# Performance work log

Hardware: AMD Instinct MI355X
Metric: run time of the kernel (lower is better)

The kernel has to match this reference:

```python
import jax, jax.numpy as jnp
import numpy as np

B, C, Q = 16, 1024, 128
XD, YD = 64, 32
D, H, HID, L = 512, 8, 2048, 6
HD = D // H
NEG = -1e9


def setup_inputs() -> dict:
    key = jax.random.key(0)
    ks = jax.random.split(key, 12)
    rn = lambda k, shape, s: jax.random.normal(k, shape, jnp.float32) * s
    return {
        "x_c": rn(ks[0], (B, C, XD), 1.0),
        "y_c": rn(ks[1], (B, C, YD), 1.0),
        "x_q": rn(ks[2], (B, Q, XD), 1.0),
        "W_val": rn(ks[3], (XD + YD, D), (XD + YD) ** -0.5),
        "b_val": jnp.zeros((D,), jnp.float32),
        "q_emb": rn(ks[4], (D,), D ** -0.5),
        "in_proj_w": rn(ks[5], (L, 3 * D, D), D ** -0.5),
        "in_proj_b": jnp.zeros((L, 3 * D), jnp.float32),
        "out_w": rn(ks[6], (L, D, D), D ** -0.5),
        "out_b": jnp.zeros((L, D), jnp.float32),
        "ln1_g": jnp.ones((L, D), jnp.float32),
        "ln1_b": jnp.zeros((L, D), jnp.float32),
        "lin1_w": rn(ks[7], (L, HID, D), D ** -0.5),
        "lin1_b": jnp.zeros((L, HID), jnp.float32),
        "lin2_w": rn(ks[8], (L, D, HID), HID ** -0.5),
        "lin2_b": jnp.zeros((L, D), jnp.float32),
        "ln2_g": jnp.ones((L, D), jnp.float32),
        "ln2_b": jnp.zeros((L, D), jnp.float32),
        "W_head": rn(ks[9], (D, YD), D ** -0.5),
        "b_head": jnp.zeros((YD,), jnp.float32),
    }


def _layernorm(x, g, b):
    mu = x.mean(-1, keepdims=True)
    var = ((x - mu) ** 2).mean(-1, keepdims=True)
    return (x - mu) * jax.lax.rsqrt(var + 1e-5) * g + b


def _forward(x_c, y_c, x_q, W_val, b_val, q_emb, in_proj_w, in_proj_b, out_w,
             out_b, ln1_g, ln1_b, lin1_w, lin1_b, lin2_w, lin2_b, ln2_g, ln2_b,
             W_head, b_head):
    bsz, c_len, _ = x_c.shape
    q_len = x_q.shape[1]
    S = c_len + q_len
    # concat y onto x; queries get zero y placeholder
    xy_c = jnp.concatenate([x_c, y_c], axis=-1)
    xy_q = jnp.concatenate([x_q, jnp.zeros((bsz, q_len, y_c.shape[-1]), x_q.dtype)], axis=-1)
    xy = jnp.concatenate([xy_c, xy_q], axis=1) @ W_val + b_val          # [B,S,D]
    xy = xy.at[:, -q_len:].add(q_emb)
    # src_mask: no one may attend to query positions (last q_len keys)
    bias = jnp.where(jnp.arange(S) >= c_len, jnp.float32(NEG), jnp.float32(0.0))  # [S] key axis

    def layer(x, p):
        ipw, ipb, ow, ob, g1, b1, w1, bb1, w2, bb2, g2, b2 = p
        qkv = x @ ipw.T + ipb                                           # [B,S,3D]
        q, k, v = jnp.split(qkv, 3, axis=-1)
        heads = lambda t: t.reshape(bsz, S, H, HD).transpose(0, 2, 1, 3)  # [B,H,S,HD]
        q, k, v = heads(q), heads(k), heads(v)
        scores = jnp.einsum('bhqd,bhkd->bhqk', q, k) / np.float32(np.sqrt(HD)) + bias
        attn = jax.nn.softmax(scores, axis=-1)
        ctx = jnp.einsum('bhqk,bhkd->bhqd', attn, v)
        ctx = ctx.transpose(0, 2, 1, 3).reshape(bsz, S, D)
        x = _layernorm(x + ctx @ ow.T + ob, g1, b1)                     # post-norm
        ff = jax.nn.relu(x @ w1.T + bb1) @ w2.T + bb2
        x = _layernorm(x + ff, g2, b2)
        return x, None

    params = (in_proj_w, in_proj_b, out_w, out_b, ln1_g, ln1_b,
              lin1_w, lin1_b, lin2_w, lin2_b, ln2_g, ln2_b)
    x, _ = jax.lax.scan(layer, xy, params)
    return x[:, -q_len:] @ W_head + b_head                              # [B,Q,YD]


def reference(x_c, y_c, x_q, W_val, b_val, q_emb, in_proj_w, in_proj_b, out_w,
              out_b, ln1_g, ln1_b, lin1_w, lin1_b, lin2_w, lin2_b, ln2_g, ln2_b,
              W_head, b_head):
    return _forward(x_c, y_c, x_q, W_val, b_val, q_emb, in_proj_w, in_proj_b,
                    out_w, out_b, ln1_g, ln1_b, lin1_w, lin1_b, lin2_w, lin2_b,
                    ln2_g, ln2_b, W_head, b_head)
```

## Files before the change

kernel.cpp:

```cpp
#include <hip/hip_runtime.h>

#define B_   16
#define C_   1024
#define Q_   128
#define S_   1152
#define D_   512
#define H_   8
#define HID_ 2048
#define L_   6
#define M_   (B_*S_)
#define MQ_  (B_*Q_)
#define QSC_ 0.18033688011f

typedef short bf16x8 __attribute__((ext_vector_type(8)));
typedef float f32x4  __attribute__((ext_vector_type(4)));
#define MFMA16(a,b,c) __builtin_amdgcn_mfma_f32_16x16x32_bf16(a,b,c,0,0,0)

__device__ __forceinline__ unsigned short f2b(float f){
  union { float f; unsigned u; } v; v.f = f;
  return (unsigned short)((v.u + 0x7FFF + ((v.u >> 16) & 1)) >> 16);
}
__device__ __forceinline__ float b2f(unsigned short u){
  return __uint_as_float((unsigned)u << 16);
}
__device__ __forceinline__ void gload16(const void* g, void* l){
  __builtin_amdgcn_global_load_lds((const __attribute__((address_space(1))) void*)g,
                                   (__attribute__((address_space(3))) void*)l, 16, 0, 0);
}
__device__ __forceinline__ float waveSum(float v){
  #pragma unroll
  for (int o = 32; o > 0; o >>= 1) v += __shfl_down(v, o, 64);
  return v;
}

__global__ __launch_bounds__(256) void f2b_kernel(
    const float* __restrict__ in, unsigned short* __restrict__ out, int n4)
{
  int i = blockIdx.x*256 + threadIdx.x;
  for (; i < n4; i += gridDim.x*256) {
    float4 v = ((const float4*)in)[i];
    ushort4 o = { f2b(v.x), f2b(v.y), f2b(v.z), f2b(v.w) };
    ((ushort4*)out)[i] = o;
  }
}

__global__ __launch_bounds__(256) void f2bq_kernel(
    const float* __restrict__ in, unsigned short* __restrict__ out, int n4)
{
  int i = blockIdx.x*256 + threadIdx.x;
  for (; i < n4; i += gridDim.x*256) {
    const int row = (i >> 7) % 1536;
    const float s = (row < 512) ? QSC_ : 1.f;
    float4 v = ((const float4*)in)[i];
    ushort4 o = { f2b(v.x*s), f2b(v.y*s), f2b(v.z*s), f2b(v.w*s) };
    ((ushort4*)out)[i] = o;
  }
}

__global__ __launch_bounds__(256) void sbias_kernel(
    const float* __restrict__ in, float* __restrict__ out)
{
  int idx = blockIdx.x*256 + threadIdx.x;
  if (idx < L_*1536) {
    int j = idx % 1536;
    out[idx] = in[idx] * (j < 512 ? QSC_ : 1.f);
  }
}

__global__ __launch_bounds__(256) void packxy_kernel(
    const float* __restrict__ x_c, const float* __restrict__ y_c,
    const float* __restrict__ x_q, unsigned short* __restrict__ XY)
{
  int idx = blockIdx.x*256 + threadIdx.x;
  const int n = M_*128;
  for (; idx < n; idx += gridDim.x*256) {
    int row = idx >> 7, col = idx & 127;
    int bb = row / S_, s = row % S_;
    float v;
    if (col < 64) {
      v = (s < C_) ? x_c[((size_t)bb*C_ + s)*64 + col]
                   : x_q[((size_t)bb*Q_ + (s - C_))*64 + col];
    } else if (col < 96) {
      v = (s < C_) ? y_c[((size_t)bb*C_ + s)*32 + (col - 64)] : 0.f;
    } else if (col == 96) {
      v = 1.f;
    } else if (col == 97) {
      v = (s >= C_) ? 1.f : 0.f;
    } else v = 0.f;
    XY[idx] = f2b(v);
  }
}

__global__ __launch_bounds__(256) void wemb_kernel(
    const float* __restrict__ W_val, const float* __restrict__ b_val,
    const float* __restrict__ q_emb, unsigned short* __restrict__ Wemb)
{
  int idx = blockIdx.x*256 + threadIdx.x;
  int nn = idx >> 7, k = idx & 127;
  float v;
  if (k < 96)       v = W_val[k*D_ + nn];
  else if (k == 96) v = b_val[nn];
  else if (k == 97) v = q_emb[nn];
  else              v = 0.f;
  Wemb[idx] = f2b(v);
}

__global__ __launch_bounds__(256) void gatherq_kernel(
    const unsigned short* __restrict__ X, unsigned short* __restrict__ Xq)
{
  int row = blockIdx.x;
  int bb = row >> 7, qi = row & 127;
  const unsigned short* src = X + ((size_t)bb*S_ + C_ + qi)*D_;
  unsigned short* dst = Xq + (size_t)row*D_;
  int tid = threadIdx.x;
  dst[tid] = src[tid];
  dst[tid + 256] = src[tid + 256];
}

#define SWZ(row) (((row) >> 1) & 3)

template<int RELU, int BOUT>
__global__ __launch_bounds__(256) void bgemm_kernel(
    const unsigned short* __restrict__ A, const unsigned short* __restrict__ W,
    const float* __restrict__ bias,
    float* __restrict__ Cf, unsigned short* __restrict__ Cb, int Nn, int Kk)
{
  __shared__ short As[2][4096];
  __shared__ short Bs[2][4096];
  int lin = blockIdx.y * gridDim.x + blockIdx.x;
  const int nwg = gridDim.x * gridDim.y;
  const int cpx = nwg >> 3;
  lin = (lin & 7) * cpx + (lin >> 3);
  const int bm = (lin / gridDim.x) * 128, bn = (lin % gridDim.x) * 128;

  const int tid = threadIdx.x;
  const int w = tid >> 6, lane = tid & 63, l15 = lane & 15, l4 = lane >> 4;
  const int wm = w >> 1, wn = w & 1;
  f32x4 acc[4][4] = {};
  const size_t strA = (size_t)Kk * 2;
  const char* Abase = (const char*)A + (size_t)bm * strA;
  const char* Wbase = (const char*)W + (size_t)bn * strA;
  const int srow = tid >> 2;
  const int schunk = (tid & 3) ^ SWZ(srow);
  const size_t soff = (size_t)srow * strA + (size_t)(schunk * 16);
  const int ldsOff = w * 1024;

#define STAGEK(K0, BUF) do { \
    const char* a0_ = Abase + soff + (size_t)(K0)*2; \
    const char* b0_ = Wbase + soff + (size_t)(K0)*2; \
    char* la_ = (char*)As + (BUF)*8192 + ldsOff; \
    char* lb_ = (char*)Bs + (BUF)*8192 + ldsOff; \
    gload16(a0_,            la_); \
    gload16(a0_ + 64*strA,  la_ + 4096); \
    gload16(b0_,            lb_); \
    gload16(b0_ + 64*strA,  lb_ + 4096); \
  } while(0)

  STAGEK(0, 0);
  const int nk = Kk >> 5;
  for (int t = 0; t < nk; t++) {
    __syncthreads();
    if (t + 1 < nk) STAGEK((t+1)*32, (t+1)&1);
    const short* AsC = (const short*)As + (t&1)*4096;
    const short* BsC = (const short*)Bs + (t&1)*4096;
    bf16x8 af[4], bfr[4];
    #pragma unroll
    for (int mf = 0; mf < 4; mf++) {
      const int ar = wm*64 + mf*16 + l15;
      af[mf] = *(const bf16x8*)(AsC + ar*32 + (l4 ^ SWZ(ar))*8);
    }
    #pragma unroll
    for (int nf = 0; nf < 4; nf++) {
      const int br = wn*64 + nf*16 + l15;
      bfr[nf] = *(const bf16x8*)(BsC + br*32 + (l4 ^ SWZ(br))*8);
    }
    #pragma unroll
    for (int mf = 0; mf < 4; mf++)
      #pragma unroll
      for (int nf = 0; nf < 4; nf++)
        acc[mf][nf] = MFMA16(af[mf], bfr[nf], acc[mf][nf]);
  }
#undef STAGEK

  #pragma unroll
  for (int mf = 0; mf < 4; mf++) {
    #pragma unroll
    for (int nf = 0; nf < 4; nf++) {
      const int ccol = bn + wn*64 + nf*16 + l15;
      const float bv = bias[ccol];
      #pragma unroll
      for (int r = 0; r < 4; r++) {
        const int rrow = bm + wm*64 + mf*16 + l4*4 + r;
        float o = acc[mf][nf][r] + bv;
        if (RELU) o = fmaxf(o, 0.f);
        if (BOUT == 1) Cb[(size_t)rrow*Nn + ccol] = f2b(o);
        else           Cf[(size_t)rrow*Nn + ccol] = o;
      }
    }
  }
}

__global__ __launch_bounds__(256) void bgemm64_kernel(
    const unsigned short* __restrict__ A, const unsigned short* __restrict__ W,
    const float* __restrict__ bias, const unsigned short* __restrict__ Rsd,
    float* __restrict__ Cf, int Nn, int Kk)
{
  __shared__ short As[3][4096];
  __shared__ short Bs[3][2048];
  int lin = blockIdx.y * gridDim.x + blockIdx.x;
  const int nwg = gridDim.x * gridDim.y;
  const int cpx = nwg >> 3;
  lin = (lin & 7) * cpx + (lin >> 3);
  const int bm = (lin / gridDim.x) * 128, bn = (lin % gridDim.x) * 64;

  const int tid = threadIdx.x;
  const int w = tid >> 6, lane = tid & 63, l15 = lane & 15, l4 = lane >> 4;
  f32x4 acc[2][4] = {};
  const size_t strA = (size_t)Kk * 2;
  const char* Abase = (const char*)A + (size_t)bm * strA;
  const char* Wbase = (const char*)W + (size_t)bn * strA;
  const int srow = tid >> 2;
  const int schunk = (tid & 3) ^ SWZ(srow);
  const size_t soff = (size_t)srow * strA + (size_t)(schunk * 16);
  const int ldsOff = w * 1024;

#define STAGEK64(K0, BUF) do { \
    const char* a0_ = Abase + soff + (size_t)(K0)*2; \
    const char* b0_ = Wbase + soff + (size_t)(K0)*2; \
    char* la_ = (char*)As + (BUF)*8192 + ldsOff; \
    char* lb_ = (char*)Bs + (BUF)*4096 + ldsOff; \
    gload16(a0_,            la_); \
    gload16(a0_ + 64*strA,  la_ + 4096); \
    gload16(b0_,            lb_); \
  } while(0)

  const int nk = Kk >> 5;
  STAGEK64(0, 0);
  STAGEK64(32, 1);
  int rb = 0;
  for (int t = 0; t < nk; t++) {
    if (t + 1 < nk) asm volatile("s_waitcnt vmcnt(3)" ::: "memory");
    else            asm volatile("s_waitcnt vmcnt(0)" ::: "memory");
    __builtin_amdgcn_s_barrier();
    __builtin_amdgcn_sched_barrier(0);
    if (t + 2 < nk) {
      int wbuf = rb + 2; if (wbuf >= 3) wbuf -= 3;
      STAGEK64((t+2)*32, wbuf);
    }
    const short* AsC = (const short*)As + rb*4096;
    const short* BsC = (const short*)Bs + rb*2048;
    bf16x8 af[2], bfr[4];
    #pragma unroll
    for (int mf = 0; mf < 2; mf++) {
      const int ar = w*32 + mf*16 + l15;
      af[mf] = *(const bf16x8*)(AsC + ar*32 + (l4 ^ SWZ(ar))*8);
    }
    #pragma unroll
    for (int nf = 0; nf < 4; nf++) {
      const int br = nf*16 + l15;
      bfr[nf] = *(const bf16x8*)(BsC + br*32 + (l4 ^ SWZ(br))*8);
    }
    #pragma unroll
    for (int mf = 0; mf < 2; mf++)
      #pragma unroll
      for (int nf = 0; nf < 4; nf++)
        acc[mf][nf] = MFMA16(af[mf], bfr[nf], acc[mf][nf]);
    rb++; if (rb >= 3) rb = 0;
  }
#undef STAGEK64

  #pragma unroll
  for (int mf = 0; mf < 2; mf++) {
    #pragma unroll
    for (int nf = 0; nf < 4; nf++) {
      const int ccol = bn + nf*16 + l15;
      const float bv = bias[ccol];
      #pragma unroll
      for (int r = 0; r < 4; r++) {
        const int rrow = bm + w*32 + mf*16 + l4*4 + r;
        float o = acc[mf][nf][r] + bv + b2f(Rsd[(size_t)rrow*Nn + ccol]);
        Cf[(size_t)rrow*Nn + ccol] = o;
      }
    }
  }
}

__global__ __launch_bounds__(256) void mattn_kernel(
    const unsigned short* __restrict__ QKV, unsigned short* __restrict__ Ctx,
    int nqt, int qoff, int orows)
{
  __shared__ short Ks[64*72];
  __shared__ short Vt[64*72];
  __shared__ short Ps[4*16*72];
  int bid = blockIdx.x;
  const int nwg = gridDim.x;
  bid = (bid & 7) * (nwg >> 3) + (bid >> 3);
  const int qt = bid % nqt;
  const int h  = (bid / nqt) % H_;
  const int bb = bid / (nqt*H_);
  const int tid = threadIdx.x;
  const int w = tid >> 6, lane = tid & 63, l15 = lane & 15, l4 = lane >> 4;

  const size_t rowQ = (size_t)bb*S_ + qoff + (size_t)qt*64 + w*16 + l15;
  const unsigned short* qp = QKV + rowQ*1536 + h*64;
  const bf16x8 qf0 = *(const bf16x8*)(qp + l4*8);
  const bf16x8 qf1 = *(const bf16x8*)(qp + 32 + l4*8);

  const unsigned short* Kg = QKV + (size_t)bb*S_*1536 + 512 + h*64;
  const unsigned short* Vg = Kg + 512;

  f32x4 ctx[4] = {};
  f32x4 lacc = {};

  const bf16x8 onesv = {(short)0x3F80,(short)0x3F80,(short)0x3F80,(short)0x3F80,
                        (short)0x3F80,(short)0x3F80,(short)0x3F80,(short)0x3F80};

  char* PsW = (char*)Ps + w*2304;

  const int skey = tid >> 3, shc = tid & 7;
  const int vp   = tid >> 3, vhc = tid & 7;

  const unsigned short* gK = Kg + (size_t)skey*1536 + shc*8;
  const unsigned short* gV = Vg + (size_t)(2*vp)*1536 + vhc*8;
  bf16x8 k0v = *(const bf16x8*)gK;
  bf16x8 k1v = *(const bf16x8*)(gK + 32*1536);
  bf16x8 c0  = *(const bf16x8*)gV;
  bf16x8 c1  = *(const bf16x8*)(gV + 1536);

  for (int kt = 0; kt < 16; kt++) {
    __syncthreads();
    *(bf16x8*)((char*)Ks + skey*144      + shc*16) = k0v;
    *(bf16x8*)((char*)Ks + (skey+32)*144 + shc*16) = k1v;
    #pragma unroll
    for (int j = 0; j < 8; j++) {
      const int hd = vhc*8 + j;
      unsigned int val = (unsigned int)(unsigned short)c0[j]
                       | ((unsigned int)(unsigned short)c1[j] << 16);
      *(unsigned int*)((char*)Vt + hd*144 + ((4*vp) ^ (vhc<<4))) = val;
    }
    __syncthreads();
    if (kt < 15) {
      const unsigned short* nK = gK + (size_t)(kt+1)*98304;
      const unsigned short* nV = gV + (size_t)(kt+1)*98304;
      k0v = *(const bf16x8*)nK;
      k1v = *(const bf16x8*)(nK + 32*1536);
      c0  = *(const bf16x8*)nV;
      c1  = *(const bf16x8*)(nV + 1536);
    }

    f32x4 sac[4] = {};
    __builtin_amdgcn_s_setprio(1);
    #pragma unroll
    for (int nf = 0; nf < 4; nf++) {
      const char* kb = (char*)Ks + (nf*16 + l15)*144 + l4*16;
      bf16x8 b0 = *(const bf16x8*)kb;
      bf16x8 b1 = *(const bf16x8*)(kb + 64);
      sac[nf] = MFMA16(qf0, b0, sac[nf]);
      sac[nf] = MFMA16(qf1, b1, sac[nf]);
    }
    __builtin_amdgcn_s_setprio(0);

    #pragma unroll
    for (int r = 0; r < 4; r++) {
      unsigned short* pw = (unsigned short*)(PsW + (l4*4 + r)*144);
      pw[ 0 + l15] = (unsigned short)(__float_as_uint(__builtin_amdgcn_exp2f(sac[0][r])) >> 16);
      pw[16 + l15] = (unsigned short)(__float_as_uint(__builtin_amdgcn_exp2f(sac[1][r])) >> 16);
      pw[32 + l15] = (unsigned short)(__float_as_uint(__builtin_amdgcn_exp2f(sac[2][r])) >> 16);
      pw[48 + l15] = (unsigned short)(__float_as_uint(__builtin_amdgcn_exp2f(sac[3][r])) >> 16);
    }

    const char* pb = PsW + l15*144 + l4*16;
    const bf16x8 pf0 = *(const bf16x8*)pb;
    const bf16x8 pf1 = *(const bf16x8*)(pb + 64);
    __builtin_amdgcn_s_setprio(1);
    lacc = MFMA16(pf0, onesv, lacc);
    lacc = MFMA16(pf1, onesv, lacc);
    #pragma unroll
    for (int hf = 0; hf < 4; hf++) {
      const int hd = hf*16 + l15;
      const int hc = (hd >> 3) & 7;
      const char* vb = (char*)Vt + hd*144;
      bf16x8 v0 = *(const bf16x8*)(vb + ((l4*16)     ^ (hc<<4)));
      bf16x8 v1 = *(const bf16x8*)(vb + (((l4+4)*16) ^ (hc<<4)));
      ctx[hf] = MFMA16(pf0, v0, ctx[hf]);
      ctx[hf] = MFMA16(pf1, v1, ctx[hf]);
    }
    __builtin_amdgcn_s_setprio(0);
  }

  #pragma unroll
  for (int r = 0; r < 4; r++) {
    const float invl = 1.0f / lacc[r];
    const size_t row = (size_t)bb*orows + (size_t)qt*64 + w*16 + l4*4 + r;
    unsigned short* op = Ctx + row*512 + h*64;
    op[ 0 + l15] = f2b(ctx[0][r]*invl);
    op[16 + l15] = f2b(ctx[1][r]*invl);
    op[32 + l15] = f2b(ctx[2][r]*invl);
    op[48 + l15] = f2b(ctx[3][r]*invl);
  }
}

__global__ __launch_bounds__(256) void ln_kernel(
    const float* __restrict__ Yin, const float* __restrict__ g, const float* __restrict__ b,
    unsigned short* __restrict__ Xb)
{
  int row = blockIdx.x, tid = threadIdx.x;
  const float* yr = Yin + (size_t)row*D_;
  float v0 = yr[tid], v1 = yr[tid + 256];
  __shared__ float red[4];
  float s = waveSum(v0 + v1);
  if ((tid & 63) == 0) red[tid >> 6] = s;
  __syncthreads();
  float mu = (red[0] + red[1] + red[2] + red[3]) * (1.f/512.f);
  __syncthreads();
  float d0 = v0 - mu, d1 = v1 - mu;
  float ss = waveSum(d0*d0 + d1*d1);
  if ((tid & 63) == 0) red[tid >> 6] = ss;
  __syncthreads();
  float inv = rsqrtf((red[0] + red[1] + red[2] + red[3]) * (1.f/512.f) + 1e-5f);
  Xb[(size_t)row*D_ + tid]       = f2b(d0 * inv * g[tid]       + b[tid]);
  Xb[(size_t)row*D_ + tid + 256] = f2b(d1 * inv * g[tid + 256] + b[tid + 256]);
}

__global__ __launch_bounds__(64) void head_kernel(
    const unsigned short* __restrict__ Xq, const float* __restrict__ W_head,
    const float* __restrict__ b_head, float* __restrict__ out)
{
  int row = blockIdx.x;
  const unsigned short* xr = Xq + (size_t)row*D_;
  __shared__ float xs[512];
  int tid = threadIdx.x;
  for (int i = tid; i < 512; i += 64) xs[i] = b2f(xr[i]);
  __syncthreads();
  if (tid < 32) {
    float acc = b_head[tid];
    #pragma unroll 8
    for (int k = 0; k < 512; k++) acc += xs[k] * W_head[k*32 + tid];
    out[(size_t)row*32 + tid] = acc;
  }
}

extern "C" void kernel_launch(void* const* d_in, const int* in_sizes, int n_in,
                              void* d_out, int out_size, void* d_ws, size_t ws_size,
                              hipStream_t stream)
{
  const float* x_c      = (const float*)d_in[0];
  const float* y_c      = (const float*)d_in[1];
  const float* x_q      = (const float*)d_in[2];
  const float* W_val    = (const float*)d_in[3];
  const float* b_val    = (const float*)d_in[4];
  const float* q_emb    = (const float*)d_in[5];
  const float* in_proj_w= (const float*)d_in[6];
  const float* in_proj_b= (const float*)d_in[7];
  const float* out_w    = (const float*)d_in[8];
  const float* out_b    = (const float*)d_in[9];
  const float* ln1_g    = (const float*)d_in[10];
  const float* ln1_b    = (const float*)d_in[11];
  const float* lin1_w   = (const float*)d_in[12];
  const float* lin1_b   = (const float*)d_in[13];
  const float* lin2_w   = (const float*)d_in[14];
  const float* lin2_b   = (const float*)d_in[15];
  const float* ln2_g    = (const float*)d_in[16];
  const float* ln2_b    = (const float*)d_in[17];
  const float* W_head   = (const float*)d_in[18];
  const float* b_head   = (const float*)d_in[19];
  float* out = (float*)d_out;

  char* p = (char*)d_ws;
  float* Yf = (float*)p;                     p += (size_t)M_*D_*4;
  unsigned short* hid  = (unsigned short*)p; p += (size_t)M_*HID_*2;
  unsigned short* Xb2  = (unsigned short*)p; p += (size_t)M_*D_*2;
  unsigned short* qkv  = (unsigned short*)p; p += (size_t)M_*3*D_*2;
  unsigned short* Xb1  = qkv;
  unsigned short* ctxb = (unsigned short*)p; p += (size_t)M_*D_*2;
  unsigned short* ipwB = (unsigned short*)p; p += (size_t)L_*3*D_*D_*2;
  unsigned short* owB  = (unsigned short*)p; p += (size_t)L_*D_*D_*2;
  unsigned short* w1B  = (unsigned short*)p; p += (size_t)L_*HID_*D_*2;
  unsigned short* w2B  = (unsigned short*)p; p += (size_t)L_*D_*HID_*2;
  unsigned short* XYb  = (unsigned short*)p; p += (size_t)M_*128*2;
  unsigned short* Wemb = (unsigned short*)p; p += (size_t)D_*128*2;
  float* zbias         = (float*)p;          p += 2048*4;
  float* qkvbias       = (float*)p;          p += L_*1536*4;

  unsigned short* ctxq  = ctxb;
  float*          Yfq   = Yf;
  unsigned short* hidq  = hid;
  unsigned short* Xqb2  = XYb;
  unsigned short* Xqb1  = XYb + (size_t)MQ_*D_;

  (void)hipMemsetAsync(zbias, 0, 2048*4, stream);

  f2bq_kernel<<<512, 256, 0, stream>>>(in_proj_w, ipwB, L_*3*D_*D_/4);
  sbias_kernel<<<36, 256, 0, stream>>>(in_proj_b, qkvbias);
  f2b_kernel<<<512, 256, 0, stream>>>(out_w,     owB,  L_*D_*D_/4);
  f2b_kernel<<<512, 256, 0, stream>>>(lin1_w,    w1B,  L_*HID_*D_/4);
  f2b_kernel<<<512, 256, 0, stream>>>(lin2_w,    w2B,  L_*D_*HID_/4);
  wemb_kernel<<<256, 256, 0, stream>>>(W_val, b_val, q_emb, Wemb);
  packxy_kernel<<<1024, 256, 0, stream>>>(x_c, y_c, x_q, XYb);

  bgemm_kernel<0,1><<<dim3(4, 144), 256, 0, stream>>>(
      XYb, Wemb, zbias, nullptr, Xb2, D_, 128);

  for (int l = 0; l < L_ - 1; l++) {
    bgemm_kernel<0,1><<<dim3(12, 144), 256, 0, stream>>>(
        Xb2, ipwB + (size_t)l*3*D_*D_, qkvbias + (size_t)l*3*D_,
        nullptr, qkv, 3*D_, D_);
    mattn_kernel<<<B_*H_*18, 256, 0, stream>>>(qkv, ctxb, 18, 0, S_);
    bgemm64_kernel<<<dim3(8, 144), 256, 0, stream>>>(
        ctxb, owB + (size_t)l*D_*D_, out_b + (size_t)l*D_, Xb2, Yf, D_, D_);
    ln_kernel<<<M_, 256, 0, stream>>>(Yf, ln1_g + (size_t)l*D_, ln1_b + (size_t)l*D_, Xb1);
    bgemm_kernel<1,1><<<dim3(16, 144), 256, 0, stream>>>(
        Xb1, w1B + (size_t)l*HID_*D_, lin1_b + (size_t)l*HID_,
        nullptr, hid, HID_, D_);
    bgemm64_kernel<<<dim3(8, 144), 256, 0, stream>>>(
        hid, w2B + (size_t)l*D_*HID_, lin2_b + (size_t)l*D_, Xb1, Yf, D_, HID_);
    ln_kernel<<<M_, 256, 0, stream>>>(Yf, ln2_g + (size_t)l*D_, ln2_b + (size_t)l*D_, Xb2);
  }

  {
    const int l = L_ - 1;
    bgemm_kernel<0,1><<<dim3(12, 144), 256, 0, stream>>>(
        Xb2, ipwB + (size_t)l*3*D_*D_, qkvbias + (size_t)l*3*D_,
        nullptr, qkv, 3*D_, D_);
    mattn_kernel<<<B_*H_*2, 256, 0, stream>>>(qkv, ctxq, 2, C_, Q_);
    gatherq_kernel<<<MQ_, 256, 0, stream>>>(Xb2, Xqb2);
    bgemm64_kernel<<<dim3(8, 16), 256, 0, stream>>>(
        ctxq, owB + (size_t)l*D_*D_, out_b + (size_t)l*D_, Xqb2, Yfq, D_, D_);
    ln_kernel<<<MQ_, 256, 0, stream>>>(Yfq, ln1_g + (size_t)l*D_, ln1_b + (size_t)l*D_, Xqb1);
    bgemm_kernel<1,1><<<dim3(16, 16), 256, 0, stream>>>(
        Xqb1, w1B + (size_t)l*HID_*D_, lin1_b + (size_t)l*HID_,
        nullptr, hidq, HID_, D_);
    bgemm64_kernel<<<dim3(8, 16), 256, 0, stream>>>(
        hidq, w2B + (size_t)l*D_*HID_, lin2_b + (size_t)l*D_, Xqb1, Yfq, D_, HID_);
    ln_kernel<<<MQ_, 256, 0, stream>>>(Yfq, ln2_g + (size_t)l*D_, ln2_b + (size_t)l*D_, Xqb2);
  }

  head_kernel<<<MQ_, 64, 0, stream>>>(Xqb2, W_head, b_head, out);
}
```

Baseline: 1.725 ms.

## Switch bgemm64 to double-buffered K=64 tiles with syncthreads pipeline

The residual GEMM kernel (bgemm64) moves from a triple-buffered K=32 pipeline with explicit vmcnt waits to a double-buffered K=64 pipeline. Each step stages a 128x64 A tile and a 64x64 W tile with a new XOR swizzle, then issues twice as many MFMAs per barrier. The aim is fewer barriers and better amortised load latency per iteration. The cost is that __syncthreads waits for all outstanding loads, so the prefetch overlaps less precisely, and LDS use grows.

After: 1.585 ms. 8.1% less time.

```diff
diff --git a/kernel.cpp b/kernel.cpp
--- a/kernel.cpp
+++ b/kernel.cpp
@@ -205,8 +205,8 @@
     const float* __restrict__ bias, const unsigned short* __restrict__ Rsd,
     float* __restrict__ Cf, int Nn, int Kk)
 {
-  __shared__ short As[3][4096];
-  __shared__ short Bs[3][2048];
+  __shared__ short As[2][8192];
+  __shared__ short Bs[2][4096];
   int lin = blockIdx.y * gridDim.x + blockIdx.x;
   const int nwg = gridDim.x * gridDim.y;
   const int cpx = nwg >> 3;
@@ -219,55 +219,59 @@
   const size_t strA = (size_t)Kk * 2;
   const char* Abase = (const char*)A + (size_t)bm * strA;
   const char* Wbase = (const char*)W + (size_t)bn * strA;
-  const int srow = tid >> 2;
-  const int schunk = (tid & 3) ^ SWZ(srow);
+  const int srow = tid >> 3;
+  const int schunk = (tid & 7) ^ (srow & 7);
   const size_t soff = (size_t)srow * strA + (size_t)(schunk * 16);
   const int ldsOff = w * 1024;
 
-#define STAGEK64(K0, BUF) do { \
+#define STG64(K0, BUF) do { \
     const char* a0_ = Abase + soff + (size_t)(K0)*2; \
     const char* b0_ = Wbase + soff + (size_t)(K0)*2; \
-    char* la_ = (char*)As + (BUF)*8192 + ldsOff; \
-    char* lb_ = (char*)Bs + (BUF)*4096 + ldsOff; \
+    char* la_ = (char*)As + (BUF)*16384 + ldsOff; \
+    char* lb_ = (char*)Bs + (BUF)*8192  + ldsOff; \
     gload16(a0_,            la_); \
-    gload16(a0_ + 64*strA,  la_ + 4096); \
+    gload16(a0_ + 32*strA,  la_ + 4096); \
+    gload16(a0_ + 64*strA,  la_ + 8192); \
+    gload16(a0_ + 96*strA,  la_ + 12288); \
     gload16(b0_,            lb_); \
+    gload16(b0_ + 32*strA,  lb_ + 4096); \
   } while(0)
 
-  const int nk = Kk >> 5;
-  STAGEK64(0, 0);
-  STAGEK64(32, 1);
-  int rb = 0;
+  STG64(0, 0);
+  const int nk = Kk >> 6;
   for (int t = 0; t < nk; t++) {
-    if (t + 1 < nk) asm volatile("s_waitcnt vmcnt(3)" ::: "memory");
-    else            asm volatile("s_waitcnt vmcnt(0)" ::: "memory");
-    __builtin_amdgcn_s_barrier();
-    __builtin_amdgcn_sched_barrier(0);
-    if (t + 2 < nk) {
-      int wbuf = rb + 2; if (wbuf >= 3) wbuf -= 3;
-      STAGEK64((t+2)*32, wbuf);
-    }
-    const short* AsC = (const short*)As + rb*4096;
-    const short* BsC = (const short*)Bs + rb*2048;
-    bf16x8 af[2], bfr[4];
+    __syncthreads();
+    if (t + 1 < nk) STG64((t+1)*64, (t+1)&1);
+    const short* AsC = (const short*)As + (t&1)*8192;
+    const short* BsC = (const short*)Bs + (t&1)*4096;
+    bf16x8 af[2][2], bfr[4][2];
     #pragma unroll
     for (int mf = 0; mf < 2; mf++) {
       const int ar = w*32 + mf*16 + l15;
-      af[mf] = *(const bf16x8*)(AsC + ar*32 + (l4 ^ SWZ(ar))*8);
+      #pragma unroll
+      for (int ks = 0; ks < 2; ks++) {
+        const int c = ks*4 + l4;
+        af[mf][ks] = *(const bf16x8*)(AsC + ar*64 + (c ^ (ar & 7))*8);
+      }
     }
     #pragma unroll
     for (int nf = 0; nf < 4; nf++) {
       const int br = nf*16 + l15;
-      bfr[nf] = *(const bf16x8*)(BsC + br*32 + (l4 ^ SWZ(br))*8);
-    }
-    #pragma unroll
-    for (int mf = 0; mf < 2; mf++)
       #pragma unroll
-      for (int nf = 0; nf < 4; nf++)
-        acc[mf][nf] = MFMA16(af[mf], bfr[nf], acc[mf][nf]);
-    rb++; if (rb >= 3) rb = 0;
-  }
-#undef STAGEK64
+      for (int ks = 0; ks < 2; ks++) {
+        const int c = ks*4 + l4;
+        bfr[nf][ks] = *(const bf16x8*)(BsC + br*64 + (c ^ (br & 7))*8);
+      }
+    }
+    #pragma unroll
+    for (int ks = 0; ks < 2; ks++)
+      #pragma unroll
+      for (int mf = 0; mf < 2; mf++)
+        #pragma unroll
+        for (int nf = 0; nf < 4; nf++)
+          acc[mf][nf] = MFMA16(af[mf][ks], bfr[nf][ks], acc[mf][nf]);
+  }
+#undef STG64
 
   #pragma unroll
   for (int mf = 0; mf < 2; mf++) {
```
